# Kernel optimization log

Hardware: AMD Instinct MI355X
Metric: run time of the kernel (lower is better)

## Reference

```python
import jax, jax.numpy as jnp
import numpy as np

D_MODEL = 512
D_STATE = 128
D_CONV = 4
EXPAND = 2
HEADDIM = 64
D_INNER = EXPAND * D_MODEL            # 1024
NHEADS = D_INNER // HEADDIM           # 16
CONV_DIM = D_INNER + 2 * D_STATE      # 1280
D_IN_PROJ = 2 * D_INNER + 2 * D_STATE + NHEADS  # 2320
EPS = 1e-5


def _mamba2(u, in_w, conv_w, conv_b, A_log, dt_bias, Dp, norm_w, out_w):
    # u: [b, l, d_model]  -- Mamba2 forward (ngroups=1), SSD in exact quadratic form
    b, l, _ = u.shape
    zxbcdt = u @ in_w.T                                   # [b,l,2320]
    z = zxbcdt[..., :D_INNER]
    xBC = zxbcdt[..., D_INNER:D_INNER + CONV_DIM]
    dt = zxbcdt[..., D_INNER + CONV_DIM:]                 # [b,l,nheads]
    # causal depthwise conv1d (kernel 4) + silu
    xp = jnp.pad(xBC, ((0, 0), (D_CONV - 1, 0), (0, 0)))
    conv = sum(xp[:, k:k + l, :] * conv_w[:, k] for k in range(D_CONV))
    xBC = jax.nn.silu(conv + conv_b)
    x = xBC[..., :D_INNER].reshape(b, l, NHEADS, HEADDIM)
    Bm = xBC[..., D_INNER:D_INNER + D_STATE]              # [b,l,d_state]
    Cm = xBC[..., D_INNER + D_STATE:]                     # [b,l,d_state]
    dt = jax.nn.softplus(dt + dt_bias)                    # [b,l,nheads]
    dtA = dt * (-jnp.exp(A_log))                          # [b,l,nheads], negative
    # SSD quadratic (semiseparable) form: L[t,s] = exp(sum_{r=s+1..t} dtA_r), causal
    cs = jnp.cumsum(dtA, axis=1)                          # [b,l,nh]
    seg = cs[:, :, None, :] - cs[:, None, :, :]           # [b,t,s,nh]
    mask = jnp.tril(jnp.ones((l, l), bool))
    L = jnp.exp(jnp.where(mask[None, :, :, None], seg, -jnp.inf))
    G = jnp.einsum('btd,bsd->bts', Cm, Bm)                # C_t . B_s
    dtx = dt[..., None] * x                               # [b,l,nh,hd]
    y = jnp.einsum('btsn,bsnp->btnp', G[..., None] * L, dtx)
    y = (y + x * Dp[:, None]).reshape(b, l, D_INNER)      # D skip
    # gated RMSNorm (norm_before_gate=False): rmsnorm(y * silu(z)) * weight
    y = y * jax.nn.silu(z)
    y = y * jax.lax.rsqrt(jnp.mean(jnp.square(y), -1, keepdims=True) + EPS) * norm_w
    return y @ out_w.T


def _forward(x, h_in_w, h_conv_w, h_conv_b, h_A_log, h_dt_bias, h_D, h_norm_w, h_out_w,
             v_in_w, v_conv_w, v_conv_b, v_A_log, v_dt_bias, v_D, v_norm_w, v_out_w,
             fc_w, fc_b):
    B, H, W, C = x.shape
    hp = (h_in_w, h_conv_w, h_conv_b, h_A_log, h_dt_bias, h_D, h_norm_w, h_out_w)
    vp = (v_in_w, v_conv_w, v_conv_b, v_A_log, v_dt_bias, v_D, v_norm_w, v_out_w)
    # horizontal: scan along W for each (B*H) row
    xh = x.reshape(-1, W, C)
    h1 = _mamba2(xh, *hp)
    # NOTE: original code flips dim 0 (batch), reproduced faithfully
    h2 = jnp.flip(_mamba2(jnp.flip(xh, 0), *hp), 0)
    h = jnp.concatenate([h1, h2], -1).reshape(B, H, W, -1)
    # vertical: scan along H for each (B*W) column
    xv = jnp.transpose(x, (0, 2, 1, 3)).reshape(-1, H, C)
    v1 = _mamba2(xv, *vp)
    v2 = jnp.flip(_mamba2(jnp.flip(xv, 0), *vp), 0)
    v = jnp.transpose(jnp.concatenate([v1, v2], -1).reshape(B, W, H, -1), (0, 2, 1, 3))
    out = jnp.concatenate([v, h], -1) @ fc_w.T + fc_b     # [B,H,W,C]
    return out


def setup_inputs() -> dict:
    key = jax.random.key(0)
    ks = jax.random.split(key, 8)
    B, H, W, C = 2, 64, 64, D_MODEL
    x = jax.random.normal(ks[0], (B, H, W, C), jnp.float32)

    def mk(k):
        kk = jax.random.split(k, 5)
        return {
            'in_w': 0.02 * jax.random.normal(kk[0], (D_IN_PROJ, D_MODEL), jnp.float32),
            'conv_w': 0.1 * jax.random.normal(kk[1], (CONV_DIM, D_CONV), jnp.float32),
            'conv_b': jnp.zeros((CONV_DIM,), jnp.float32),
            'A_log': jnp.log(jax.random.uniform(kk[2], (NHEADS,), jnp.float32, 1.0, 16.0)),
            'dt_bias': jnp.log(jnp.expm1(jax.random.uniform(kk[3], (NHEADS,), jnp.float32, 1e-3, 0.1))),
            'D': jnp.ones((NHEADS,), jnp.float32),
            'norm_w': jnp.ones((D_INNER,), jnp.float32),
            'out_w': 0.02 * jax.random.normal(kk[4], (D_MODEL, D_INNER), jnp.float32),
        }

    hp, vp = mk(ks[1]), mk(ks[2])
    inp = {'x': x}
    inp.update({f'h_{n}': v for n, v in hp.items()})
    inp.update({f'v_{n}': v for n, v in vp.items()})
    inp['fc_w'] = 0.02 * jax.random.normal(ks[3], (D_MODEL, 4 * D_MODEL), jnp.float32)
    inp['fc_b'] = jnp.zeros((D_MODEL,), jnp.float32)
    return inp


def reference(x, h_in_w, h_conv_w, h_conv_b, h_A_log, h_dt_bias, h_D, h_norm_w, h_out_w,
              v_in_w, v_conv_w, v_conv_b, v_A_log, v_dt_bias, v_D, v_norm_w, v_out_w,
              fc_w, fc_b):
    return _forward(x, h_in_w, h_conv_w, h_conv_b, h_A_log, h_dt_bias, h_D, h_norm_w, h_out_w,
                    v_in_w, v_conv_w, v_conv_b, v_A_log, v_dt_bias, v_D, v_norm_w, v_out_w,
                    fc_w, fc_b)
```

## Files before the change

kernel.cpp:

```cpp
#include <hip/hip_runtime.h>

#define NROWS 8192
#define NZX   2304
#define BCS   136
#define XMS   72

#define PB0 4096
#define PB1 (PB0 + 2048)
#define PB2 (PB1 + 2304)
#define PB3 (PB2 + 256)
#define PB4 (PB3 + 512)

typedef __attribute__((ext_vector_type(8))) short bf16x8;
typedef __attribute__((ext_vector_type(4))) float f32x4;

__device__ __forceinline__ float bf2f(unsigned short u) {
    union { unsigned int i; float f; } v; v.i = ((unsigned int)u) << 16; return v.f;
}
__device__ __forceinline__ unsigned short f2bf(float f) {
    union { float f; unsigned int i; } v; v.f = f;
    return (unsigned short)((v.i + 0x8000u) >> 16);
}

__device__ __forceinline__ void async_lds16(const unsigned short* g, unsigned short* l) {
    __builtin_amdgcn_global_load_lds(
        (const __attribute__((address_space(1))) unsigned int*)g,
        (__attribute__((address_space(3))) unsigned int*)l, 16, 0, 0);
}

__global__ __launch_bounds__(256) void prep_kernel(
    const float* __restrict__ x, const float* __restrict__ fcw,
    const float* __restrict__ iw0, const float* __restrict__ iw1,
    const float* __restrict__ ow0, const float* __restrict__ ow1,
    const float* __restrict__ db0, const float* __restrict__ db1,
    const float* __restrict__ al0, const float* __restrict__ al1,
    unsigned short* __restrict__ xbf, unsigned short* __restrict__ wf,
    unsigned short* __restrict__ wbA, unsigned short* __restrict__ wbOT0,
    unsigned short* __restrict__ wbOT1, float* __restrict__ dtbb,
    float* __restrict__ csbb)
{
    __shared__ char sm[37888] __attribute__((aligned(16)));
    const int blk = blockIdx.x, tid = threadIdx.x;
    if (blk < PB0) {
        int i = blk * 256 + tid;
        float4 v = *(const float4*)(x + (size_t)i * 4);
        ushort4 o;
        o.x = f2bf(v.x); o.y = f2bf(v.y); o.z = f2bf(v.z); o.w = f2bf(v.w);
        *(ushort4*)(xbf + (size_t)i * 4) = o;
    } else if (blk < PB1) {
        int idx = (blk - PB0) * 256 + tid;
        int o = idx >> 10, c = idx & 1023;
        int half = c >> 9, cc = c & 511;
        float v = fcw[(size_t)o * 2048 + half * 1024 + cc] +
                  fcw[(size_t)o * 2048 + half * 1024 + 512 + cc];
        wf[idx] = f2bf(v);
    } else if (blk < PB2) {
        int local = blk - PB1;
        int dir = local / 1152;
        int i = (local % 1152) * 256 + tid;
        const float* s = dir ? iw1 : iw0;
        float4 v = *(const float4*)(s + (size_t)i * 4);
        ushort4 o;
        o.x = f2bf(v.x); o.y = f2bf(v.y); o.z = f2bf(v.z); o.w = f2bf(v.w);
        *(ushort4*)(wbA + (size_t)dir * (2304 * 512) + (size_t)i * 4) = o;
    } else if (blk < PB3) {
        float (*T)[65] = (float(*)[65])sm;
        int local = blk - PB2;
        int z = local >> 7, rem = local & 127;
        const float* s = z ? ow1 : ow0;
        unsigned short* d = z ? wbOT1 : wbOT0;
        const int bo = (rem >> 4) * 64, bc = (rem & 15) * 64;
#pragma unroll
        for (int i = 0; i < 16; ++i) {
            int slot = tid + i * 256;
            int r = slot >> 6, c = slot & 63;
            T[r][c] = s[(size_t)(bo + r) * 1024 + bc + c];
        }
        __syncthreads();
#pragma unroll
        for (int i = 0; i < 16; ++i) {
            int slot = tid + i * 256;
            int cr = slot >> 6, oc = slot & 63;
            d[(size_t)(bc + cr) * 512 + bo + oc] = f2bf(T[oc][cr]);
        }
    } else {
        float (*wsm)[512] = (float(*)[512])sm;
        float (*xs)[68]   = (float(*)[68])(sm + 16384);
        float (*dta)[64]  = (float(*)[64])(sm + 16384 + 17408);
        float (*dtt)[64]  = (float(*)[64])(sm + 16384 + 17408 + 2048);
        int local = blk - PB3;
        const int dir = local >> 8, bxl = local & 255;
        const float* in_w = dir ? iw1 : iw0;
        const float* dt_bias = dir ? db1 : db0;
        const float* A_log = dir ? al1 : al0;
        float* dtb = dtbb + (size_t)dir * 131072;
        float* csb = csbb + (size_t)dir * 131072;
        const int seq = bxl >> 1, hq = bxl & 1;
#pragma unroll
        for (int i = 0; i < 4; ++i) {
            int slot = tid + i * 256;
            int h = slot >> 7, c = (slot & 127) * 4;
            *(float4*)&wsm[h][c] = *(const float4*)(in_w + (size_t)(2304 + hq * 8 + h) * 512 + c);
        }
        const int t = tid & 63, hg = tid >> 6;
        float acc[2] = {0.f, 0.f};
        for (int c0 = 0; c0 < 512; c0 += 64) {
            __syncthreads();
#pragma unroll
            for (int i = 0; i < 4; ++i) {
                int slot = tid + i * 256;
                int r = slot >> 4, cc = (slot & 15) * 4;
                size_t row = (dir == 0) ? (size_t)seq * 64 + r
                                        : (size_t)(seq >> 6) * 4096 + (size_t)r * 64 + (seq & 63);
                *(float4*)&xs[r][cc] = *(const float4*)(x + row * 512 + c0 + cc);
            }
            __syncthreads();
#pragma unroll
            for (int cc = 0; cc < 64; cc += 4) {
                float4 u4 = *(const float4*)&xs[t][cc];
                const float* w0 = &wsm[hg * 2][c0 + cc];
                const float* w1 = &wsm[hg * 2 + 1][c0 + cc];
                acc[0] += u4.x * w0[0] + u4.y * w0[1] + u4.z * w0[2] + u4.w * w0[3];
                acc[1] += u4.x * w1[0] + u4.y * w1[1] + u4.z * w1[2] + u4.w * w1[3];
            }
        }
#pragma unroll
        for (int hh = 0; hh < 2; ++hh) {
            int hl = hg * 2 + hh;
            int h = hq * 8 + hl;
            float v = acc[hh] + dt_bias[h];
            float dtv = (v > 20.f) ? v : log1pf(__expf(v));
            dtt[hl][t] = dtv;
            dta[hl][t] = dtv * -__expf(A_log[h]);
        }
        __syncthreads();
        if (tid < 8) {
            float run = 0.f;
            int ob = (seq * 16 + hq * 8 + tid) * 64;
            for (int tt = 0; tt < 64; ++tt) {
                run += dta[tid][tt];
                dtb[ob + tt] = dtt[tid][tt];
                csb[ob + tt] = run;
            }
        }
    }
}

__global__ __launch_bounds__(256) void gemm_phase(
    const unsigned short* __restrict__ xbf, const unsigned short* __restrict__ wbA,
    unsigned short* __restrict__ zx, const unsigned short* __restrict__ wf,
    const unsigned short* __restrict__ wbOT0, const unsigned short* __restrict__ wbOT1,
    unsigned short* __restrict__ wcomb, const float* __restrict__ cw0,
    const float* __restrict__ cw1, const float* __restrict__ cb0,
    const float* __restrict__ cb1, unsigned short* __restrict__ xbc)
{
    __shared__ unsigned short SMEM[16384];
    unsigned short* As = SMEM;
    unsigned short* Bs = SMEM + 8192;
    const int bx = blockIdx.x, by = blockIdx.y, z = blockIdx.z;
    const int inproj = (by < 18);
    const unsigned short *A, *B;
    unsigned short* C;
    int lda, ldb, ldc, perm, mB, nB;
    if (inproj) {
        int did = by * 64 + bx;
        int xcd = did & 7, l = did >> 3;
        mB = (xcd * 8 + (l & 7)) * 128;
        nB = (l >> 3) * 128;
        A = xbf; lda = 512; perm = z;
        B = wbA + (size_t)z * (2304 * 512); ldb = 512;
        C = zx + (size_t)z * NROWS * NZX; ldc = NZX;
    } else {
        if (bx >= 32) return;
        A = z ? wf : wf + 512; lda = 1024; perm = 0;
        B = z ? wbOT1 : wbOT0; ldb = 512;
        C = z ? wcomb : wcomb + 1024; ldc = 2048;
        mB = (bx >> 3) * 128; nB = (bx & 7) * 128;
    }
    const int tid = threadIdx.x, wave = tid >> 6, lane = tid & 63;
    const int wm = (wave >> 1) * 64, wn = (wave & 1) * 64;
    const int lr = lane & 15, lq = lane >> 4;
    const unsigned short* AgP[4];
    const unsigned short* BgP[4];
    unsigned short* lA[4];
    unsigned short* lB[4];
#pragma unroll
    for (int i = 0; i < 4; ++i) {
        int s = tid + i * 256;
        int r = s >> 3, p = s & 7;
        int q = p ^ (r & 7);
        int ar = mB + r;
        if (perm) ar = (ar & ~4095) | ((ar & 63) << 6) | ((ar >> 6) & 63);
        AgP[i] = A + (size_t)ar * lda + q * 8;
        BgP[i] = B + (size_t)(nB + r) * ldb + q * 8;
        lA[i] = As + s * 8;
        lB[i] = Bs + s * 8;
    }
    const int aswz = lr & 7;
    int arb[4], brb[4];
#pragma unroll
    for (int i = 0; i < 4; ++i) {
        arb[i] = (wm + i * 16 + lr) * 64;
        brb[i] = (wn + i * 16 + lr) * 64;
    }
    f32x4 zero4 = {0.f,0.f,0.f,0.f};
    f32x4 acc[4][4] = {{zero4,zero4,zero4,zero4},{zero4,zero4,zero4,zero4},
                       {zero4,zero4,zero4,zero4},{zero4,zero4,zero4,zero4}};
    for (int k0 = 0; k0 < 512; k0 += 64) {
#pragma unroll
        for (int i = 0; i < 4; ++i) async_lds16(AgP[i] + k0, lA[i]);
#pragma unroll
        for (int i = 0; i < 4; ++i) async_lds16(BgP[i] + k0, lB[i]);
        __syncthreads();
#pragma unroll
        for (int kh = 0; kh < 2; ++kh) {
            const int ksw = ((kh * 4 + lq) ^ aswz) * 8;
            bf16x8 a[4], b[4];
#pragma unroll
            for (int i = 0; i < 4; ++i) a[i] = *(const bf16x8*)(As + arb[i] + ksw);
#pragma unroll
            for (int i = 0; i < 4; ++i) b[i] = *(const bf16x8*)(Bs + brb[i] + ksw);
#pragma unroll
            for (int mi = 0; mi < 4; ++mi)
#pragma unroll
                for (int ni = 0; ni < 4; ++ni)
                    acc[mi][ni] = __builtin_amdgcn_mfma_f32_16x16x32_bf16(
                        a[mi], b[ni], acc[mi][ni], 0, 0, 0);
        }
        __syncthreads();
    }
    if (inproj && nB >= 1024) {
        const int ch0 = (nB - 1024) + wn;
        const float* cwp = z ? cw1 : cw0;
        const float* cbp = z ? cb1 : cb0;
        float4 wv[4]; float bb[4];
#pragma unroll
        for (int ni = 0; ni < 4; ++ni) {
            int c = ch0 + ni * 16 + lr;
            wv[ni] = *(const float4*)(cwp + (size_t)c * 4);
            bb[ni] = cbp[c];
        }
        const int rsl = (lane + 48) & 63;
        unsigned short* WR = SMEM + wave * 1024;
        unsigned short* xo = xbc + (size_t)z * NROWS * 1280
                           + (size_t)(mB + wm) * 1280;
        float pr1[4] = {0.f,0.f,0.f,0.f};
        float pr2[4] = {0.f,0.f,0.f,0.f};
        float pr3[4] = {0.f,0.f,0.f,0.f};
#pragma unroll
        for (int mi = 0; mi < 4; ++mi) {
#pragma unroll
            for (int ni = 0; ni < 4; ++ni) {
                float vq[4];
#pragma unroll
                for (int r = 0; r < 4; ++r) vq[r] = bf2f(f2bf(acc[mi][ni][r]));
                float rc1 = __shfl(vq[1], rsl);
                float rc2 = __shfl(vq[2], rsl);
                float rc3 = __shfl(vq[3], rsl);
                float u1 = lq ? rc3 : pr3[ni];
                float u2 = lq ? rc2 : pr2[ni];
                float u3 = lq ? rc1 : pr1[ni];
                pr1[ni] = rc1; pr2[ni] = rc2; pr3[ni] = rc3;
                float y4[4];
                y4[0] = bb[ni] + wv[ni].w*vq[0] + wv[ni].z*u1    + wv[ni].y*u2    + wv[ni].x*u3;
                y4[1] = bb[ni] + wv[ni].w*vq[1] + wv[ni].z*vq[0] + wv[ni].y*u1    + wv[ni].x*u2;
                y4[2] = bb[ni] + wv[ni].w*vq[2] + wv[ni].z*vq[1] + wv[ni].y*vq[0] + wv[ni].x*u1;
                y4[3] = bb[ni] + wv[ni].w*vq[3] + wv[ni].z*vq[2] + wv[ni].y*vq[1] + wv[ni].x*vq[0];
#pragma unroll
                for (int r = 0; r < 4; ++r) {
                    float a = y4[r];
                    float s = a / (1.f + __expf(-a));
                    int r16 = lq * 4 + r;
                    int cn = ni * 16 + lr;
                    int gp = ((cn >> 3) + (r16 >> 1)) & 7;
                    WR[r16 * 64 + gp * 8 + (cn & 7)] = f2bf(s);
                }
            }
#pragma unroll
            for (int j = 0; j < 2; ++j) {
                int r16 = j * 8 + (lane >> 3);
                int gr = lane & 7;
                int gp = (gr + (r16 >> 1)) & 7;
                uint4 v = *(const uint4*)(WR + r16 * 64 + gp * 8);
                *(uint4*)(xo + (size_t)(mi * 16 + r16) * 1280 + ch0 + gr * 8) = v;
            }
        }
    } else {
        unsigned short* WR = SMEM + wave * 1024;
#pragma unroll
        for (int mi = 0; mi < 4; ++mi) {
#pragma unroll
            for (int ni = 0; ni < 4; ++ni) {
#pragma unroll
                for (int r = 0; r < 4; ++r) {
                    int r16 = lq * 4 + r;
                    int cn = ni * 16 + lr;
                    int gp = ((cn >> 3) + (r16 >> 1)) & 7;
                    WR[r16 * 64 + gp * 8 + (cn & 7)] = f2bf(acc[mi][ni][r]);
                }
            }
#pragma unroll
            for (int j = 0; j < 2; ++j) {
                int r16 = j * 8 + (lane >> 3);
                int gr = lane & 7;
                int gp = (gr + (r16 >> 1)) & 7;
                uint4 v = *(const uint4*)(WR + r16 * 64 + gp * 8);
                int row = mB + wm + mi * 16 + r16;
                *(uint4*)(C + (size_t)row * ldc + nB + wn + gr * 8) = v;
            }
        }
    }
}

__global__ __launch_bounds__(256) void gemm_final2048(
    const unsigned short* __restrict__ YV, const unsigned short* __restrict__ YH,
    const unsigned short* __restrict__ W, const float* __restrict__ bias,
    float* __restrict__ C)
{
    __shared__ unsigned short As[128 * 64];
    __shared__ unsigned short Bs[64 * 64];
    const int tid = threadIdx.x, wave = tid >> 6, lane = tid & 63;
    const int did = blockIdx.y * 64 + blockIdx.x;
    const int mB = (did >> 3) * 128, nB = (did & 7) * 64;
    const int lr = lane & 15, lq = lane >> 4;
    int aq[4], agr[4], apr[4];
    unsigned short* lA[4];
    const unsigned short* BgP[2];
    unsigned short* lB[2];
#pragma unroll
    for (int i = 0; i < 4; ++i) {
        int s = tid + i * 256;
        int r = s >> 3, p = s & 7;
        aq[i] = (p ^ (r & 7)) * 8;
        int gr = mB + r;
        agr[i] = gr;
        apr[i] = (gr & ~4095) | ((gr & 63) << 6) | ((gr >> 6) & 63);
        lA[i] = As + s * 8;
    }
#pragma unroll
    for (int i = 0; i < 2; ++i) {
        int s = tid + i * 256;
        int r = s >> 3, p = s & 7;
        int q = p ^ (r & 7);
        BgP[i] = W + (size_t)(nB + r) * 2048 + q * 8;
        lB[i] = Bs + s * 8;
    }
    const int aswz = lr & 7;
    int arb[2], brb[4];
#pragma unroll
    for (int i = 0; i < 2; ++i) arb[i] = (wave * 32 + i * 16 + lr) * 64;
#pragma unroll
    for (int i = 0; i < 4; ++i) brb[i] = (i * 16 + lr) * 64;
    f32x4 zero4 = {0.f,0.f,0.f,0.f};
    f32x4 acc[2][4] = {{zero4,zero4,zero4,zero4},{zero4,zero4,zero4,zero4}};
    for (int k0 = 0; k0 < 2048; k0 += 64) {
#pragma unroll
        for (int i = 0; i < 4; ++i) {
            int kk = k0 + aq[i];
            const unsigned short* g = (kk < 1024)
                ? YV + (size_t)apr[i] * 1024 + kk
                : YH + (size_t)agr[i] * 1024 + (kk - 1024);
            async_lds16(g, lA[i]);
        }
#pragma unroll
        for (int i = 0; i < 2; ++i) async_lds16(BgP[i] + k0, lB[i]);
        __syncthreads();
#pragma unroll
        for (int kh = 0; kh < 2; ++kh) {
            const int ksw = ((kh * 4 + lq) ^ aswz) * 8;
            bf16x8 a[2], b[4];
#pragma unroll
            for (int i = 0; i < 2; ++i) a[i] = *(const bf16x8*)(As + arb[i] + ksw);
#pragma unroll
            for (int i = 0; i < 4; ++i) b[i] = *(const bf16x8*)(Bs + brb[i] + ksw);
#pragma unroll
            for (int mi = 0; mi < 2; ++mi)
#pragma unroll
                for (int ni = 0; ni < 4; ++ni)
                    acc[mi][ni] = __builtin_amdgcn_mfma_f32_16x16x32_bf16(
                        a[mi], b[ni], acc[mi][ni], 0, 0, 0);
        }
        __syncthreads();
    }
    const int rbase = lq * 4;
#pragma unroll
    for (int mi = 0; mi < 2; ++mi)
#pragma unroll
        for (int ni = 0; ni < 4; ++ni) {
            int col = nB + ni * 16 + lr;
            float bb = bias[col];
#pragma unroll
            for (int r = 0; r < 4; ++r) {
                int row = mB + wave * 32 + mi * 16 + rbase + r;
                C[(size_t)row * 512 + col] = acc[mi][ni][r] + bb;
            }
        }
}

__global__ __launch_bounds__(256) void gmat_kernel(
    const unsigned short* __restrict__ xbcb, float* __restrict__ Gbuf)
{
    __shared__ unsigned short Bs[64 * BCS];
    __shared__ unsigned short Cs[64 * BCS];
    const int dir = blockIdx.y, seq = blockIdx.x;
    const unsigned short* base = xbcb + (size_t)dir * NROWS * 1280
                                      + (size_t)seq * 64 * 1280;
    const int tid = threadIdx.x;
    const int lane = tid & 63, wave = tid >> 6;
#pragma unroll
    for (int i = 0; i < 4; ++i) {
        int e = (tid + i * 256) * 8;
        int r = e >> 7, c = e & 127;
        *(uint4*)(Bs + r * BCS + c) = *(const uint4*)(base + (size_t)r * 1280 + 1024 + c);
        *(uint4*)(Cs + r * BCS + c) = *(const uint4*)(base + (size_t)r * 1280 + 1152 + c);
    }
    __syncthreads();
    const int lr = lane & 15, lq = lane >> 4;
    f32x4 zero4 = {0.f,0.f,0.f,0.f};
    f32x4 acc[4] = {zero4, zero4, zero4, zero4};
#pragma unroll
    for (int kt = 0; kt < 4; ++kt) {
        bf16x8 a = *(const bf16x8*)(Cs + (wave * 16 + lr) * BCS + kt * 32 + lq * 8);
#pragma unroll
        for (int ni = 0; ni < 4; ++ni) {
            bf16x8 b = *(const bf16x8*)(Bs + (ni * 16 + lr) * BCS + kt * 32 + lq * 8);
            acc[ni] = __builtin_amdgcn_mfma_f32_16x16x32_bf16(a, b, acc[ni], 0, 0, 0);
        }
    }
    float* G = Gbuf + ((size_t)dir * 128 + seq) * 4096;
#pragma unroll
    for (int ni = 0; ni < 4; ++ni) {
        int s = ni * 16 + lr;
#pragma unroll
        for (int r = 0; r < 4; ++r) {
            int t = wave * 16 + lq * 4 + r;
            G[t * 64 + s] = acc[ni][r];
        }
    }
}

__global__ __launch_bounds__(256) void scan_kernel(
    const unsigned short* __restrict__ xbcb, const float* __restrict__ Gbuf,
    const float* __restrict__ dtbb, const float* __restrict__ csbb,
    const float* __restrict__ Dv0, const float* __restrict__ Dv1,
    unsigned short* __restrict__ yh, unsigned short* __restrict__ yv)
{
    __shared__ unsigned short XsT[64 * XMS];
    __shared__ unsigned short Ms[64 * XMS];
    __shared__ float dts[64], css[64];
    const int dir = blockIdx.y;
    const unsigned short* xbc = xbcb + (size_t)dir * NROWS * 1280;
    const float* dtb = dtbb + (size_t)dir * 131072;
    const float* csb = csbb + (size_t)dir * 131072;
    const float* Dv = dir ? Dv1 : Dv0;
    unsigned short* y = dir ? yv : yh;
    const int tid = threadIdx.x;
    const int lane = tid & 63, wave = tid >> 6;
    const int seq = blockIdx.x >> 4, h = blockIdx.x & 15;
    if (tid < 64) {
        dts[tid] = dtb[(seq * 16 + h) * 64 + tid];
        css[tid] = csb[(seq * 16 + h) * 64 + tid];
    }
    const unsigned short* base = xbc + (size_t)seq * 64 * 1280;
#pragma unroll
    for (int i = 0; i < 2; ++i) {
        int e = (tid + i * 256) * 8;
        int t = e >> 6, p0 = e & 63;
        uint4 xval = *(const uint4*)(base + (size_t)t * 1280 + h * 64 + p0);
        const unsigned short* xs = (const unsigned short*)&xval;
#pragma unroll
        for (int j = 0; j < 8; ++j) {
            int jl = (j + lane) & 7;
            XsT[(p0 + jl) * XMS + t] = xs[jl];
        }
    }
    const int lr = lane & 15, lq = lane >> 4;
    const float* G = Gbuf + ((size_t)dir * 128 + seq) * 4096;
    f32x4 acc[4];
#pragma unroll
    for (int ni = 0; ni < 4; ++ni) {
        int s = ni * 16 + lr;
#pragma unroll
        for (int r = 0; r < 4; ++r) {
            int t = wave * 16 + lq * 4 + r;
            acc[ni][r] = G[t * 64 + s];
        }
    }
    __syncthreads();
    float css_t[4];
#pragma unroll
    for (int r = 0; r < 4; ++r) css_t[r] = css[wave * 16 + lq * 4 + r];
#pragma unroll
    for (int ni = 0; ni < 4; ++ni) {
        int s = ni * 16 + lr;
        float cs_s = css[s], dt_s = dts[s];
#pragma unroll
        for (int r = 0; r < 4; ++r) {
            int t = wave * 16 + lq * 4 + r;
            float e = __expf(fminf(css_t[r] - cs_s, 0.f));
            float m = (s <= t) ? acc[ni][r] * e * dt_s : 0.f;
            Ms[t * XMS + s] = f2bf(m);
        }
    }
    __syncthreads();
    f32x4 zero4 = {0.f,0.f,0.f,0.f};
    f32x4 yacc[4] = {zero4, zero4, zero4, zero4};
#pragma unroll
    for (int kt = 0; kt < 2; ++kt) {
        bf16x8 a = *(const bf16x8*)(Ms + (wave * 16 + lr) * XMS + kt * 32 + lq * 8);
#pragma unroll
        for (int ni = 0; ni < 4; ++ni) {
            bf16x8 b = *(const bf16x8*)(XsT + (ni * 16 + lr) * XMS + kt * 32 + lq * 8);
            yacc[ni] = __builtin_amdgcn_mfma_f32_16x16x32_bf16(a, b, yacc[ni], 0, 0, 0);
        }
    }
    const float Dh = Dv[h];
#pragma unroll
    for (int ni = 0; ni < 4; ++ni) {
        int p = ni * 16 + lr;
#pragma unroll
        for (int r = 0; r < 4; ++r) {
            int t = wave * 16 + lq * 4 + r;
            float v = yacc[ni][r] + Dh * bf2f(XsT[p * XMS + t]);
            Ms[t * XMS + p] = f2bf(v);
        }
    }
    __syncthreads();
    unsigned short* yout = y + (size_t)seq * 64 * 1024 + h * 64;
#pragma unroll
    for (int i = 0; i < 2; ++i) {
        int slot = tid + i * 256;
        int t = slot >> 3, pc = (slot & 7) * 8;
        uint4 v = *(const uint4*)(Ms + t * XMS + pc);
        *(uint4*)(yout + (size_t)t * 1024 + pc) = v;
    }
}

__global__ __launch_bounds__(128) void gate_norm(
    const unsigned short* __restrict__ zxb, unsigned short* __restrict__ yh,
    unsigned short* __restrict__ yv, const float* __restrict__ nw0,
    const float* __restrict__ nw1)
{
    const int dir = blockIdx.y;
    const unsigned short* zx = zxb + (size_t)dir * NROWS * NZX;
    unsigned short* y = dir ? yv : yh;
    const float* nw = dir ? nw1 : nw0;
    const int row = blockIdx.x, tid = threadIdx.x;
    uint4 yv4 = *(const uint4*)(y + (size_t)row * 1024 + tid * 8);
    uint4 zv4 = *(const uint4*)(zx + (size_t)row * NZX + tid * 8);
    const unsigned short* ys = (const unsigned short*)&yv4;
    const unsigned short* zs = (const unsigned short*)&zv4;
    float g[8]; float ss = 0.f;
#pragma unroll
    for (int j = 0; j < 8; ++j) {
        float zv = bf2f(zs[j]);
        float gv = bf2f(ys[j]) * (zv / (1.f + __expf(-zv)));
        g[j] = gv; ss += gv * gv;
    }
#pragma unroll
    for (int off = 32; off > 0; off >>= 1) ss += __shfl_xor(ss, off, 64);
    __shared__ float red[2];
    if ((tid & 63) == 0) red[tid >> 6] = ss;
    __syncthreads();
    ss = red[0] + red[1];
    const float scale = rsqrtf(ss * (1.f / 1024.f) + 1e-5f);
    unsigned short out8[8] __attribute__((aligned(16)));
#pragma unroll
    for (int j = 0; j < 8; ++j) out8[j] = f2bf(g[j] * scale * nw[tid * 8 + j]);
    *(uint4*)(y + (size_t)row * 1024 + tid * 8) = *(const uint4*)out8;
}

extern "C" void kernel_launch(void* const* d_in, const int* in_sizes, int n_in,
                              void* d_out, int out_size, void* d_ws, size_t ws_size,
                              hipStream_t stream)
{
    (void)in_sizes; (void)n_in; (void)out_size; (void)ws_size;
    const float* x   = (const float*)d_in[0];
    const float* fcw = (const float*)d_in[17];
    const float* fcb = (const float*)d_in[18];
    const float* iw0 = (const float*)d_in[1];  const float* iw1 = (const float*)d_in[9];
    const float* cw0 = (const float*)d_in[2];  const float* cw1 = (const float*)d_in[10];
    const float* cb0 = (const float*)d_in[3];  const float* cb1 = (const float*)d_in[11];
    const float* al0 = (const float*)d_in[4];  const float* al1 = (const float*)d_in[12];
    const float* db0 = (const float*)d_in[5];  const float* db1 = (const float*)d_in[13];
    const float* Dv0 = (const float*)d_in[6];  const float* Dv1 = (const float*)d_in[14];
    const float* nw0 = (const float*)d_in[7];  const float* nw1 = (const float*)d_in[15];
    const float* ow0 = (const float*)d_in[8];  const float* ow1 = (const float*)d_in[16];

    char* ws = (char*)d_ws;
    size_t off = 0;
    auto alloc = [&](size_t bytes) {
        void* p = ws + off; off += (bytes + 255) & ~(size_t)255; return p;
    };
    unsigned short* xbf   = (unsigned short*)alloc((size_t)NROWS * 512 * 2);
    unsigned short* wbA   = (unsigned short*)alloc((size_t)2 * 2304 * 512 * 2);
    unsigned short* wbOT0 = (unsigned short*)alloc((size_t)1024 * 512 * 2);
    unsigned short* wbOT1 = (unsigned short*)alloc((size_t)1024 * 512 * 2);
    unsigned short* wf    = (unsigned short*)alloc((size_t)512 * 1024 * 2);
    unsigned short* wcomb = (unsigned short*)alloc((size_t)512 * 2048 * 2);
    unsigned short* zx    = (unsigned short*)alloc((size_t)2 * NROWS * NZX * 2);
    unsigned short* xbc   = (unsigned short*)alloc((size_t)2 * NROWS * 1280 * 2);
    float* Gbuf           = (float*)alloc((size_t)2 * 128 * 4096 * 4);
    float* dtb            = (float*)alloc((size_t)2 * 2048 * 64 * 4);
    float* csb            = (float*)alloc((size_t)2 * 2048 * 64 * 4);
    unsigned short* ybh   = (unsigned short*)alloc((size_t)NROWS * 1024 * 2);
    unsigned short* ybv   = (unsigned short*)alloc((size_t)NROWS * 1024 * 2);

    prep_kernel<<<PB4, 256, 0, stream>>>(x, fcw, iw0, iw1, ow0, ow1, db0, db1,
                                         al0, al1, xbf, wf, wbA, wbOT0, wbOT1,
                                         dtb, csb);
    gemm_phase<<<dim3(64, 19, 2), 256, 0, stream>>>(xbf, wbA, zx, wf,
                                                    wbOT0, wbOT1, wcomb,
                                                    cw0, cw1, cb0, cb1, xbc);
    gmat_kernel<<<dim3(128, 2), 256, 0, stream>>>(xbc, Gbuf);
    scan_kernel<<<dim3(2048, 2), 256, 0, stream>>>(xbc, Gbuf, dtb, csb,
                                                   Dv0, Dv1, ybh, ybv);
    gate_norm<<<dim3(NROWS, 2), 128, 0, stream>>>(zx, ybh, ybv, nw0, nw1);
    gemm_final2048<<<dim3(64, 8), 256, 0, stream>>>(ybv, ybh, wcomb, fcb, (float*)d_out);
}
```

Before: 283.3 us.

## Rewrite projection GEMM with 256x256 tiles, 512 threads and double-buffered LDS pipeline

Replaces the 128x128-tile, 256-thread projection GEMM with a 256x256-tile, 8-wave kernel. The kernel double-buffers LDS and interleaves the async loads for the next k-step with four MFMA sub-phases, raising MFMA priority during compute. The aim is more data reuse per tile and hiding global-load latency behind MFMA work. In exchange it uses 128KB of LDS and more accumulator registers, which lowers occupancy. The grid shrinks to 296 blocks per z, which may leave some CUs idle. The conv epilogue now skips the bf16 rounding of accumulators.

```diff
diff --git a/kernel.cpp b/kernel.cpp
--- a/kernel.cpp
+++ b/kernel.cpp
@@ -146,7 +146,37 @@
     }
 }
 
-__global__ __launch_bounds__(256) void gemm_phase(
+struct GemmEpi { unsigned short* C; int ldc; int colsub; int conv; };
+
+template<int QA, int QB>
+__device__ __forceinline__ void phase_mma(
+    const unsigned short* AS, const unsigned short* BS, int cb,
+    const int (&aoff)[4], const int (&boff)[2], const int (&kcx)[2],
+    f32x4 (&acc)[8][4])
+{
+    const unsigned short* Ab = AS + cb * 16384 + QA * 8192;
+    const unsigned short* Bb = BS + cb * 16384 + QB * 8192;
+    bf16x8 av[2][4], bv[2][2];
+#pragma unroll
+    for (int kh = 0; kh < 2; ++kh) {
+#pragma unroll
+        for (int f = 0; f < 4; ++f) av[kh][f] = *(const bf16x8*)(Ab + aoff[f] + kcx[kh]);
+#pragma unroll
+        for (int g = 0; g < 2; ++g) bv[kh][g] = *(const bf16x8*)(Bb + boff[g] + kcx[kh]);
+    }
+    __builtin_amdgcn_s_setprio(1);
+#pragma unroll
+    for (int f = 0; f < 4; ++f)
+#pragma unroll
+        for (int g = 0; g < 2; ++g)
+#pragma unroll
+            for (int kh = 0; kh < 2; ++kh)
+                acc[QA * 4 + f][QB * 2 + g] = __builtin_amdgcn_mfma_f32_16x16x32_bf16(
+                    av[kh][f], bv[kh][g], acc[QA * 4 + f][QB * 2 + g], 0, 0, 0);
+    __builtin_amdgcn_s_setprio(0);
+}
+
+__global__ __launch_bounds__(512) void gemm_big(
     const unsigned short* __restrict__ xbf, const unsigned short* __restrict__ wbA,
     unsigned short* __restrict__ zx, const unsigned short* __restrict__ wf,
     const unsigned short* __restrict__ wbOT0, const unsigned short* __restrict__ wbOT1,
@@ -154,162 +184,178 @@
     const float* __restrict__ cw1, const float* __restrict__ cb0,
     const float* __restrict__ cb1, unsigned short* __restrict__ xbc)
 {
-    __shared__ unsigned short SMEM[16384];
-    unsigned short* As = SMEM;
-    unsigned short* Bs = SMEM + 8192;
-    const int bx = blockIdx.x, by = blockIdx.y, z = blockIdx.z;
-    const int inproj = (by < 18);
+    __shared__ unsigned short SMEM[65536] __attribute__((aligned(16)));
+    unsigned short* AS = SMEM;
+    unsigned short* BS = SMEM + 32768;
+    const int bx = blockIdx.x, z = blockIdx.z;
     const unsigned short *A, *B;
-    unsigned short* C;
-    int lda, ldb, ldc, perm, mB, nB;
-    if (inproj) {
-        int did = by * 64 + bx;
-        int xcd = did & 7, l = did >> 3;
-        mB = (xcd * 8 + (l & 7)) * 128;
-        nB = (l >> 3) * 128;
+    int lda, perm, mB, nB;
+    GemmEpi epi;
+    if (bx < 288) {
+        int xcd = bx & 7, l = bx >> 3;
+        int cid = xcd * 36 + l;
+        int mt = cid / 9, nt = cid - mt * 9;
+        mB = mt * 256; nB = nt * 256;
         A = xbf; lda = 512; perm = z;
-        B = wbA + (size_t)z * (2304 * 512); ldb = 512;
-        C = zx + (size_t)z * NROWS * NZX; ldc = NZX;
+        B = wbA + (size_t)z * (2304 * 512);
+        if (nB >= 1024) { epi.C = xbc + (size_t)z * NROWS * 1280; epi.ldc = 1280; epi.colsub = 1024; epi.conv = 1; }
+        else            { epi.C = zx + (size_t)z * NROWS * NZX;  epi.ldc = NZX;  epi.colsub = 0;    epi.conv = 0; }
     } else {
-        if (bx >= 32) return;
+        int t2 = bx - 288;
+        mB = (t2 >> 2) * 256; nB = (t2 & 3) * 256;
         A = z ? wf : wf + 512; lda = 1024; perm = 0;
-        B = z ? wbOT1 : wbOT0; ldb = 512;
-        C = z ? wcomb : wcomb + 1024; ldc = 2048;
-        mB = (bx >> 3) * 128; nB = (bx & 7) * 128;
+        B = z ? wbOT1 : wbOT0;
+        epi.C = z ? wcomb : wcomb + 1024; epi.ldc = 2048; epi.colsub = 0; epi.conv = 0;
     }
     const int tid = threadIdx.x, wave = tid >> 6, lane = tid & 63;
-    const int wm = (wave >> 1) * 64, wn = (wave & 1) * 64;
+    const int wr = wave >> 2, wc = wave & 3;
     const int lr = lane & 15, lq = lane >> 4;
-    const unsigned short* AgP[4];
-    const unsigned short* BgP[4];
-    unsigned short* lA[4];
-    unsigned short* lB[4];
-#pragma unroll
-    for (int i = 0; i < 4; ++i) {
-        int s = tid + i * 256;
-        int r = s >> 3, p = s & 7;
-        int q = p ^ (r & 7);
-        int ar = mB + r;
-        if (perm) ar = (ar & ~4095) | ((ar & 63) << 6) | ((ar >> 6) & 63);
-        AgP[i] = A + (size_t)ar * lda + q * 8;
-        BgP[i] = B + (size_t)(nB + r) * ldb + q * 8;
-        lA[i] = As + s * 8;
-        lB[i] = Bs + s * 8;
-    }
-    const int aswz = lr & 7;
-    int arb[4], brb[4];
-#pragma unroll
-    for (int i = 0; i < 4; ++i) {
-        arb[i] = (wm + i * 16 + lr) * 64;
-        brb[i] = (wn + i * 16 + lr) * 64;
-    }
-    f32x4 zero4 = {0.f,0.f,0.f,0.f};
-    f32x4 acc[4][4] = {{zero4,zero4,zero4,zero4},{zero4,zero4,zero4,zero4},
-                       {zero4,zero4,zero4,zero4},{zero4,zero4,zero4,zero4}};
-    for (int k0 = 0; k0 < 512; k0 += 64) {
-#pragma unroll
-        for (int i = 0; i < 4; ++i) async_lds16(AgP[i] + k0, lA[i]);
-#pragma unroll
-        for (int i = 0; i < 4; ++i) async_lds16(BgP[i] + k0, lB[i]);
-        __syncthreads();
-#pragma unroll
-        for (int kh = 0; kh < 2; ++kh) {
-            const int ksw = ((kh * 4 + lq) ^ aswz) * 8;
-            bf16x8 a[4], b[4];
-#pragma unroll
-            for (int i = 0; i < 4; ++i) a[i] = *(const bf16x8*)(As + arb[i] + ksw);
-#pragma unroll
-            for (int i = 0; i < 4; ++i) b[i] = *(const bf16x8*)(Bs + brb[i] + ksw);
-#pragma unroll
-            for (int mi = 0; mi < 4; ++mi)
-#pragma unroll
-                for (int ni = 0; ni < 4; ++ni)
-                    acc[mi][ni] = __builtin_amdgcn_mfma_f32_16x16x32_bf16(
-                        a[mi], b[ni], acc[mi][ni], 0, 0, 0);
-        }
-        __syncthreads();
-    }
-    if (inproj && nB >= 1024) {
-        const int ch0 = (nB - 1024) + wn;
-        const float* cwp = z ? cw1 : cw0;
-        const float* cbp = z ? cb1 : cb0;
+    const unsigned short* gA[2][2];
+    const unsigned short* gB[2][2];
+    int ldsSlot[2];
+#pragma unroll
+    for (int i = 0; i < 2; ++i) {
+        int s = tid + i * 512;
+        int r = s >> 3, p = s & 7, q = p ^ (r & 7);
+        ldsSlot[i] = s * 8;
+#pragma unroll
+        for (int h = 0; h < 2; ++h) {
+            int ar = mB + h * 128 + r;
+            if (perm) ar = (ar & ~4095) | ((ar & 63) << 6) | ((ar >> 6) & 63);
+            gA[i][h] = A + (size_t)ar * lda + q * 8;
+            gB[i][h] = B + (size_t)(nB + h * 128 + r) * 512 + q * 8;
+        }
+    }
+    int aoff[4], boff[2], kcx[2];
+#pragma unroll
+    for (int f = 0; f < 4; ++f) aoff[f] = (wr * 64 + f * 16 + lr) * 64;
+#pragma unroll
+    for (int g = 0; g < 2; ++g) boff[g] = (wc * 32 + g * 16 + lr) * 64;
+#pragma unroll
+    for (int kh = 0; kh < 2; ++kh) kcx[kh] = ((kh * 4 + lq) ^ (lr & 7)) * 8;
+    f32x4 acc[8][4];
+#pragma unroll
+    for (int m = 0; m < 8; ++m)
+#pragma unroll
+        for (int n = 0; n < 4; ++n) acc[m][n] = (f32x4){0.f, 0.f, 0.f, 0.f};
+
+#define STAGE_A(H, K0, CB) { _Pragma("unroll") \
+    for (int i = 0; i < 2; ++i) async_lds16(gA[i][H] + (K0), AS + (CB) * 16384 + (H) * 8192 + ldsSlot[i]); }
+#define STAGE_B(H, K0, CB) { _Pragma("unroll") \
+    for (int i = 0; i < 2; ++i) async_lds16(gB[i][H] + (K0), BS + (CB) * 16384 + (H) * 8192 + ldsSlot[i]); }
+
+    STAGE_A(0, 0, 0); STAGE_B(0, 0, 0); STAGE_A(1, 0, 0); STAGE_B(1, 0, 0);
+#pragma unroll 1
+    for (int t = 0; t < 7; ++t) {
+        const int cb = t & 1, nb2 = cb ^ 1, k1 = (t + 1) * 64;
+        asm volatile("s_waitcnt vmcnt(4)" ::: "memory");
+        asm volatile("s_barrier" ::: "memory");
+        STAGE_A(0, k1, nb2);
+        phase_mma<0, 0>(AS, BS, cb, aoff, boff, kcx, acc);
+        asm volatile("s_waitcnt vmcnt(4)" ::: "memory");
+        asm volatile("s_barrier" ::: "memory");
+        STAGE_B(0, k1, nb2);
+        phase_mma<1, 0>(AS, BS, cb, aoff, boff, kcx, acc);
+        asm volatile("s_waitcnt vmcnt(4)" ::: "memory");
+        asm volatile("s_barrier" ::: "memory");
+        STAGE_A(1, k1, nb2);
+        phase_mma<0, 1>(AS, BS, cb, aoff, boff, kcx, acc);
+        STAGE_B(1, k1, nb2);
+        phase_mma<1, 1>(AS, BS, cb, aoff, boff, kcx, acc);
+    }
+    asm volatile("s_waitcnt vmcnt(0)" ::: "memory");
+    asm volatile("s_barrier" ::: "memory");
+    phase_mma<0, 0>(AS, BS, 1, aoff, boff, kcx, acc);
+    phase_mma<1, 0>(AS, BS, 1, aoff, boff, kcx, acc);
+    phase_mma<0, 1>(AS, BS, 1, aoff, boff, kcx, acc);
+    phase_mma<1, 1>(AS, BS, 1, aoff, boff, kcx, acc);
+
+    unsigned short* WR = BS + wave * 1024;
+    const int rsl = (lane + 48) & 63;
+    if (epi.conv) {
         float4 wv[4]; float bb[4];
 #pragma unroll
-        for (int ni = 0; ni < 4; ++ni) {
-            int c = ch0 + ni * 16 + lr;
-            wv[ni] = *(const float4*)(cwp + (size_t)c * 4);
-            bb[ni] = cbp[c];
-        }
-        const int rsl = (lane + 48) & 63;
-        unsigned short* WR = SMEM + wave * 1024;
-        unsigned short* xo = xbc + (size_t)z * NROWS * 1280
-                           + (size_t)(mB + wm) * 1280;
-        float pr1[4] = {0.f,0.f,0.f,0.f};
-        float pr2[4] = {0.f,0.f,0.f,0.f};
-        float pr3[4] = {0.f,0.f,0.f,0.f};
-#pragma unroll
-        for (int mi = 0; mi < 4; ++mi) {
-#pragma unroll
-            for (int ni = 0; ni < 4; ++ni) {
-                float vq[4];
-#pragma unroll
-                for (int r = 0; r < 4; ++r) vq[r] = bf2f(f2bf(acc[mi][ni][r]));
-                float rc1 = __shfl(vq[1], rsl);
-                float rc2 = __shfl(vq[2], rsl);
-                float rc3 = __shfl(vq[3], rsl);
-                float u1 = lq ? rc3 : pr3[ni];
-                float u2 = lq ? rc2 : pr2[ni];
-                float u3 = lq ? rc1 : pr1[ni];
-                pr1[ni] = rc1; pr2[ni] = rc2; pr3[ni] = rc3;
-                float y4[4];
-                y4[0] = bb[ni] + wv[ni].w*vq[0] + wv[ni].z*u1    + wv[ni].y*u2    + wv[ni].x*u3;
-                y4[1] = bb[ni] + wv[ni].w*vq[1] + wv[ni].z*vq[0] + wv[ni].y*u1    + wv[ni].x*u2;
-                y4[2] = bb[ni] + wv[ni].w*vq[2] + wv[ni].z*vq[1] + wv[ni].y*vq[0] + wv[ni].x*u1;
-                y4[3] = bb[ni] + wv[ni].w*vq[3] + wv[ni].z*vq[2] + wv[ni].y*vq[1] + wv[ni].x*vq[0];
-#pragma unroll
-                for (int r = 0; r < 4; ++r) {
-                    float a = y4[r];
-                    float s = a / (1.f + __expf(-a));
-                    int r16 = lq * 4 + r;
-                    int cn = ni * 16 + lr;
-                    int gp = ((cn >> 3) + (r16 >> 1)) & 7;
-                    WR[r16 * 64 + gp * 8 + (cn & 7)] = f2bf(s);
+        for (int c4 = 0; c4 < 4; ++c4) {
+            int col = nB - 1024 + (c4 >> 1) * 128 + wc * 32 + (c4 & 1) * 16 + lr;
+            const float* cwp = z ? cw1 : cw0;
+            const float* cbp = z ? cb1 : cb0;
+            wv[c4] = *(const float4*)(cwp + (size_t)col * 4);
+            bb[c4] = cbp[col];
+        }
+#pragma unroll
+        for (int h = 0; h < 2; ++h) {
+            float pr1[4], pr2[4], pr3[4];
+#pragma unroll
+            for (int c4 = 0; c4 < 4; ++c4) { pr1[c4] = 0.f; pr2[c4] = 0.f; pr3[c4] = 0.f; }
+#pragma unroll
+            for (int f = 0; f < 4; ++f) {
+#pragma unroll
+                for (int c4 = 0; c4 < 4; ++c4) {
+                    float vq[4];
+#pragma unroll
+                    for (int r = 0; r < 4; ++r) vq[r] = acc[h * 4 + f][c4][r];
+                    float rc1 = __shfl(vq[1], rsl);
+                    float rc2 = __shfl(vq[2], rsl);
+                    float rc3 = __shfl(vq[3], rsl);
+                    float u1 = lq ? rc3 : pr3[c4];
+                    float u2 = lq ? rc2 : pr2[c4];
+                    float u3 = lq ? rc1 : pr1[c4];
+                    pr1[c4] = rc1; pr2[c4] = rc2; pr3[c4] = rc3;
+                    float y4[4];
+                    y4[0] = bb[c4] + wv[c4].w*vq[0] + wv[c4].z*u1    + wv[c4].y*u2    + wv[c4].x*u3;
+                    y4[1] = bb[c4] + wv[c4].w*vq[1] + wv[c4].z*vq[0] + wv[c4].y*u1    + wv[c4].x*u2;
+                    y4[2] = bb[c4] + wv[c4].w*vq[2] + wv[c4].z*vq[1] + wv[c4].y*vq[0] + wv[c4].x*u1;
+                    y4[3] = bb[c4] + wv[c4].w*vq[3] + wv[c4].z*vq[2] + wv[c4].y*vq[1] + wv[c4].x*vq[0];
+#pragma unroll
+                    for (int r = 0; r < 4; ++r) {
+                        float a = y4[r];
+                        float s = a / (1.f + __expf(-a));
+                        int r16 = lq * 4 + r;
+                        int cn = c4 * 16 + lr;
+                        int gp = ((cn >> 3) + (r16 >> 1)) & 7;
+                        WR[r16 * 64 + gp * 8 + (cn & 7)] = f2bf(s);
+                    }
+                }
+#pragma unroll
+                for (int j = 0; j < 2; ++j) {
+                    int r16 = j * 8 + (lane >> 3);
+                    int gr = lane & 7;
+                    int gp = (gr + (r16 >> 1)) & 7;
+                    uint4 v = *(const uint4*)(WR + r16 * 64 + gp * 8);
+                    int row = mB + h * 128 + wr * 64 + f * 16 + r16;
+                    int col = nB - epi.colsub + (gr >> 2) * 128 + wc * 32 + ((gr >> 1) & 1) * 16 + (gr & 1) * 8;
+                    *(uint4*)(epi.C + (size_t)row * epi.ldc + col) = v;
                 }
             }
-#pragma unroll
-            for (int j = 0; j < 2; ++j) {
-                int r16 = j * 8 + (lane >> 3);
-                int gr = lane & 7;
-                int gp = (gr + (r16 >> 1)) & 7;
-                uint4 v = *(const uint4*)(WR + r16 * 64 + gp * 8);
-                *(uint4*)(xo + (size_t)(mi * 16 + r16) * 1280 + ch0 + gr * 8) = v;
-            }
         }
     } else {
-        unsigned short* WR = SMEM + wave * 1024;
-#pragma unroll
-        for (int mi = 0; mi < 4; ++mi) {
-#pragma unroll
-            for (int ni = 0; ni < 4; ++ni) {
-#pragma unroll
-                for (int r = 0; r < 4; ++r) {
-                    int r16 = lq * 4 + r;
-                    int cn = ni * 16 + lr;
-                    int gp = ((cn >> 3) + (r16 >> 1)) & 7;
-                    WR[r16 * 64 + gp * 8 + (cn & 7)] = f2bf(acc[mi][ni][r]);
+#pragma unroll
+        for (int h = 0; h < 2; ++h)
+#pragma unroll
+            for (int f = 0; f < 4; ++f) {
+#pragma unroll
+                for (int c4 = 0; c4 < 4; ++c4)
+#pragma unroll
+                    for (int r = 0; r < 4; ++r) {
+                        int r16 = lq * 4 + r;
+                        int cn = c4 * 16 + lr;
+                        int gp = ((cn >> 3) + (r16 >> 1)) & 7;
+                        WR[r16 * 64 + gp * 8 + (cn & 7)] = f2bf(acc[h * 4 + f][c4][r]);
+                    }
+#pragma unroll
+                for (int j = 0; j < 2; ++j) {
+                    int r16 = j * 8 + (lane >> 3);
+                    int gr = lane & 7;
+                    int gp = (gr + (r16 >> 1)) & 7;
+                    uint4 v = *(const uint4*)(WR + r16 * 64 + gp * 8);
+                    int row = mB + h * 128 + wr * 64 + f * 16 + r16;
+                    int col = nB + (gr >> 2) * 128 + wc * 32 + ((gr >> 1) & 1) * 16 + (gr & 1) * 8;
+                    *(uint4*)(epi.C + (size_t)row * epi.ldc + col) = v;
                 }
             }
-#pragma unroll
-            for (int j = 0; j < 2; ++j) {
-                int r16 = j * 8 + (lane >> 3);
-                int gr = lane & 7;
-                int gp = (gr + (r16 >> 1)) & 7;
-                uint4 v = *(const uint4*)(WR + r16 * 64 + gp * 8);
-                int row = mB + wm + mi * 16 + r16;
-                *(uint4*)(C + (size_t)row * ldc + nB + wn + gr * 8) = v;
-            }
-        }
-    }
+    }
+#undef STAGE_A
+#undef STAGE_B
 }
 
 __global__ __launch_bounds__(256) void gemm_final2048(
@@ -609,9 +655,9 @@
     prep_kernel<<<PB4, 256, 0, stream>>>(x, fcw, iw0, iw1, ow0, ow1, db0, db1,
                                          al0, al1, xbf, wf, wbA, wbOT0, wbOT1,
                                          dtb, csb);
-    gemm_phase<<<dim3(64, 19, 2), 256, 0, stream>>>(xbf, wbA, zx, wf,
-                                                    wbOT0, wbOT1, wcomb,
-                                                    cw0, cw1, cb0, cb1, xbc);
+    gemm_big<<<dim3(296, 1, 2), 512, 0, stream>>>(xbf, wbA, zx, wf,
+                                                  wbOT0, wbOT1, wcomb,
+                                                  cw0, cw1, cb0, cb1, xbc);
     gmat_kernel<<<dim3(128, 2), 256, 0, stream>>>(xbc, Gbuf);
     scan_kernel<<<dim3(2048, 2), 256, 0, stream>>>(xbc, Gbuf, dtb, csb,
                                                    Dv0, Dv1, ybh, ybv);
```

New measurement: 282.7 us. No clear change (-0.2%).
